# Performance work log

Hardware: AMD Instinct MI355X
Metric: run time of the kernel (lower is better)

## Reference

```python
import jax, jax.numpy as jnp
import numpy as np

N_AGT, N_CTX, E, D, NC = 100000, 10000, 1000000, 128, 2


def _gn(x, w, b, eps=1e-5):
    # GroupNorm(num_groups=1) on (N, C): normalize over channels, affine.
    m = jnp.mean(x, axis=-1, keepdims=True)
    v = jnp.mean((x - m) ** 2, axis=-1, keepdims=True)
    return (x - m) * jax.lax.rsqrt(v + eps) * w + b


def setup_inputs() -> dict:
    key = jax.random.key(0)
    ks = jax.random.split(key, 16)
    s = 0.05  # weight scale
    return {
        "agts": jax.random.normal(ks[0], (N_AGT, D), jnp.float32),
        "ctx": jax.random.normal(ks[1], (N_CTX, D), jnp.float32),
        "agt_ctrs": jax.random.normal(ks[2], (N_AGT, NC), jnp.float32),
        "ctx_ctrs": jax.random.normal(ks[3], (N_CTX, NC), jnp.float32),
        "hi": jax.random.randint(ks[4], (E,), 0, N_AGT, jnp.int32),
        "wi": jax.random.randint(ks[5], (E,), 0, N_CTX, jnp.int32),
        "dist_w1": jax.random.normal(ks[6], (D, NC), jnp.float32) * s,
        "dist_b1": jnp.zeros((D,), jnp.float32),
        "dist_w2": jax.random.normal(ks[7], (D, D), jnp.float32) * s,
        "dist_gw": jnp.ones((D,), jnp.float32),
        "dist_gb": jnp.zeros((D,), jnp.float32),
        "q_w": jax.random.normal(ks[8], (D, D), jnp.float32) * s,
        "q_gw": jnp.ones((D,), jnp.float32),
        "q_gb": jnp.zeros((D,), jnp.float32),
        "ctx_w1": jax.random.normal(ks[9], (D, 3 * D), jnp.float32) * s,
        "ctx_gw": jnp.ones((D,), jnp.float32),
        "ctx_gb": jnp.zeros((D,), jnp.float32),
        "ctx_w2": jax.random.normal(ks[10], (D, D), jnp.float32) * s,
        "agt_w": jax.random.normal(ks[11], (D, D), jnp.float32) * s,
        "norm_gw": jnp.ones((D,), jnp.float32),
        "norm_gb": jnp.zeros((D,), jnp.float32),
        "lin_w": jax.random.normal(ks[12], (D, D), jnp.float32) * s,
        "lin_gw": jnp.ones((D,), jnp.float32),
        "lin_gb": jnp.zeros((D,), jnp.float32),
    }


def reference(agts, ctx, agt_ctrs, ctx_ctrs, hi, wi,
              dist_w1, dist_b1, dist_w2, dist_gw, dist_gb,
              q_w, q_gw, q_gb,
              ctx_w1, ctx_gw, ctx_gb, ctx_w2,
              agt_w, norm_gw, norm_gb,
              lin_w, lin_gw, lin_gb):
    res = agts
    # per-edge relative displacement: [E, 2]
    d = agt_ctrs[hi] - ctx_ctrs[wi]
    # dist MLP: Linear(2,128)+ReLU, Linear(128,128,nobias)+GN+ReLU
    d = jax.nn.relu(d @ dist_w1.T + dist_b1)
    d = jax.nn.relu(_gn(d @ dist_w2.T, dist_gw, dist_gb))
    # query: Linear(128,128,nobias)+GN+ReLU on gathered agents
    q = jax.nn.relu(_gn(agts[hi] @ q_w.T, q_gw, q_gb))
    # concat-MLP over edges: [E, 384] -> [E, 128]
    c = jnp.concatenate([d, q, ctx[wi]], axis=1)
    c = jax.nn.relu(_gn(c @ ctx_w1.T, ctx_gw, ctx_gb))
    c = c @ ctx_w2.T
    # agent transform + index_add scatter of edge messages
    a = agts @ agt_w.T
    a = a.at[hi].add(c)
    a = jax.nn.relu(_gn(a, norm_gw, norm_gb))
    a = _gn(a @ lin_w.T, lin_gw, lin_gb)  # Linear block with act=False
    a = jax.nn.relu(a + res)
    return a
```

## Files before the change

kernel.cpp:

```cpp
#include <hip/hip_runtime.h>
#include <stdint.h>


#define N_AGT 100000
#define N_CTX 10000
#define NE    1000000
#define D     128

typedef __attribute__((ext_vector_type(8))) __bf16 bf16x8;
typedef __attribute__((ext_vector_type(4))) float f32x4;
typedef __attribute__((ext_vector_type(4))) unsigned int uint32x4;
typedef __attribute__((ext_vector_type(8))) unsigned short ushort8;

__device__ __forceinline__ float bf_lo(uint32_t u){ return __uint_as_float(u << 16); }
__device__ __forceinline__ float bf_hi(uint32_t u){ return __uint_as_float(u & 0xFFFF0000u); }
__device__ __forceinline__ uint16_t f2bf(float f){
  uint32_t u = __float_as_uint(f);
  u += 0x7FFFu + ((u >> 16) & 1u);
  return (uint16_t)(u >> 16);
}
__device__ __forceinline__ float bf2f(uint16_t v){ return __uint_as_float(((uint32_t)v) << 16); }

__device__ __forceinline__ f32x4 mfma16(bf16x8 a, bf16x8 b, f32x4 c){
  return __builtin_amdgcn_mfma_f32_16x16x32_bf16(a, b, c, 0, 0, 0);
}

__device__ __forceinline__ void wave_lgkm0(){
  asm volatile("s_waitcnt lgkmcnt(0)" ::: "memory");
  __builtin_amdgcn_sched_barrier(0);
}


__device__ __forceinline__ void stage_wsz(char* dst, const float* __restrict__ W,
                                          int rs, int co, int tid, int nthr){
  for (int idx = tid; idx < 128*16; idx += nthr){
    const int row = idx >> 4, ch = idx & 15;
    const float4 f0 = *(const float4*)(W + (size_t)row*rs + co + ch*8);
    const float4 f1 = *(const float4*)(W + (size_t)row*rs + co + ch*8 + 4);
    ushort8 u;
    u[0]=f2bf(f0.x); u[1]=f2bf(f0.y); u[2]=f2bf(f0.z); u[3]=f2bf(f0.w);
    u[4]=f2bf(f1.x); u[5]=f2bf(f1.y); u[6]=f2bf(f1.z); u[7]=f2bf(f1.w);
    *(uint32x4*)(dst + row*256 + ((ch*16) ^ ((row&7)<<4))) = __builtin_bit_cast(uint32x4, u);
  }
}

__device__ __forceinline__ bf16x8 ldfrag(const char* base, int row, int cb){
  return __builtin_bit_cast(bf16x8,
      *(const uint32x4*)(base + row*256 + (cb ^ ((row&7)<<4))));
}

__global__ __launch_bounds__(256) void k_hist(const int* __restrict__ hi,
                                              int* __restrict__ cnt){
  for (int i = blockIdx.x*256 + threadIdx.x; i < NE; i += gridDim.x*256)
    atomicAdd(&cnt[hi[i]], 1);
}

__global__ __launch_bounds__(1024) void k_scan(int* __restrict__ cnt){
  __shared__ int part[1024];
  const int t = threadIdx.x;
  const int chunk = (N_AGT + 1023) / 1024;
  const int lo = t*chunk, hi2 = min(lo + chunk, N_AGT);
  int s = 0;
  for (int i = lo; i < hi2; i++) s += cnt[i];
  part[t] = s;
  __syncthreads();
  for (int ofs = 1; ofs < 1024; ofs <<= 1){
    int add = (t >= ofs) ? part[t - ofs] : 0;
    __syncthreads();
    part[t] += add;
    __syncthreads();
  }
  int run = part[t] - s;
  for (int i = lo; i < hi2; i++){
    const int c = cnt[i];
    cnt[i] = run;
    run += c;
  }
}

__global__ __launch_bounds__(256) void k_scatter(const int* __restrict__ hi,
                                                 const int* __restrict__ wi,
                                                 int* __restrict__ cur,
                                                 int* __restrict__ hs,
                                                 int* __restrict__ ws){
  for (int i = blockIdx.x*256 + threadIdx.x; i < NE; i += gridDim.x*256){
    const int h = hi[i];
    const int pos = atomicAdd(&cur[h], 1);
    hs[pos] = h;
    ws[pos] = wi[i];
  }
}

#define NWIT (NE/16)

__device__ __forceinline__ void mm16(const char* T, const char* W,
                                     int llo, int lhi, f32x4 acc[8]){
  bf16x8 a[4];
  #pragma unroll
  for (int kt = 0; kt < 4; kt++) a[kt] = ldfrag(T, llo, kt*64 + lhi*16);
  #pragma unroll
  for (int nt = 0; nt < 8; nt++){
    acc[nt] = (f32x4)0.f;
    #pragma unroll
    for (int kt = 0; kt < 4; kt++){
      const bf16x8 b = ldfrag(W, nt*16 + llo, kt*64 + lhi*16);
      acc[nt] = mfma16(a[kt], b, acc[nt]);
    }
  }
}

__device__ __forceinline__ void gn_reg(f32x4 acc[8], const float gw[8],
                                       const float gb[8]){
  float s[4] = {0,0,0,0}, ss[4] = {0,0,0,0};
  #pragma unroll
  for (int nt = 0; nt < 8; nt++)
    #pragma unroll
    for (int r = 0; r < 4; r++){
      const float v = acc[nt][r];
      s[r] += v; ss[r] += v*v;
    }
  #pragma unroll
  for (int m = 1; m < 16; m <<= 1)
    #pragma unroll
    for (int r = 0; r < 4; r++){
      s[r] += __shfl_xor(s[r], m);
      ss[r] += __shfl_xor(ss[r], m);
    }
  float mean[4], rstd[4];
  #pragma unroll
  for (int r = 0; r < 4; r++){
    mean[r] = s[r]*(1.f/128.f);
    const float var = ss[r]*(1.f/128.f) - mean[r]*mean[r];
    rstd[r] = rsqrtf(var + 1e-5f);
  }
  #pragma unroll
  for (int nt = 0; nt < 8; nt++)
    #pragma unroll
    for (int r = 0; r < 4; r++)
      acc[nt][r] = fmaxf((acc[nt][r]-mean[r])*rstd[r]*gw[nt] + gb[nt], 0.f);
}

__device__ __forceinline__ void scat16(char* T, const f32x4 acc[8],
                                       int llo, int lhi){
  #pragma unroll
  for (int nt = 0; nt < 8; nt++)
    #pragma unroll
    for (int r = 0; r < 4; r++){
      const int row = lhi*4 + r;
      *(uint16_t*)(T + row*256 + ((2*(nt*16 + llo)) ^ ((row&7)<<4))) =
          f2bf(acc[nt][r]);
    }
}

__global__ __launch_bounds__(512, 2) void k_edge_mfma(
    const float* __restrict__ agt_ctrs, const float* __restrict__ ctx_ctrs,
    const int* __restrict__ hs, const int* __restrict__ ws,
    const float* __restrict__ dist_w1, const float* __restrict__ dist_b1,
    const float* __restrict__ dist_gw, const float* __restrict__ dist_gb,
    const float* __restrict__ ctx_gw, const float* __restrict__ ctx_gb,
    const float* __restrict__ dist_w2, const float* __restrict__ ctx_w1,
    const float* __restrict__ ctx_w2,
    const uint16_t* __restrict__ QW, const uint16_t* __restrict__ CtxP,
    float* __restrict__ A0){
  extern __shared__ __align__(16) char smem[];
  const int tid  = threadIdx.x;
  const int wave = tid >> 6, lane = tid & 63;
  const int lhi  = lane >> 4, llo = lane & 15;

  stage_wsz(smem,         dist_w2, 128, 0, tid, 512);
  stage_wsz(smem + 32768, ctx_w1,  384, 0, tid, 512);
  stage_wsz(smem + 65536, ctx_w2,  128, 0, tid, 512);

  char* T = smem + 98304 + wave*4096;

  const int c0 = llo*8;
  float w1x[8], w1y[8], b1v[8];
  #pragma unroll
  for (int j = 0; j < 8; j++){
    w1x[j] = dist_w1[(c0+j)*2 + 0];
    w1y[j] = dist_w1[(c0+j)*2 + 1];
    b1v[j] = dist_b1[c0+j];
  }
  float dgwr[8], dgbr[8], cgwr[8], cgbr[8];
  #pragma unroll
  for (int nt = 0; nt < 8; nt++){
    dgwr[nt] = dist_gw[nt*16 + llo]; dgbr[nt] = dist_gb[nt*16 + llo];
    cgwr[nt] = ctx_gw[nt*16 + llo];  cgbr[nt] = ctx_gb[nt*16 + llo];
  }
  __syncthreads();

  const int wid = blockIdx.x*8 + wave;
  const int nw  = gridDim.x*8;

  for (int i = wid; i < NWIT; i += nw){
    const int base = i*16;
    const int4 h4 = *(const int4*)&hs[base + lhi*4];
    const int4 w4 = *(const int4*)&ws[base + lhi*4];
    const int hh[4] = {h4.x, h4.y, h4.z, h4.w};
    const int ww[4] = {w4.x, w4.y, w4.z, w4.w};
    const int h2 = hs[base + llo], w2 = ws[base + llo];
    uint32x4 qql[4], qcl[4];
    #pragma unroll
    for (int k = 0; k < 4; k++){
      qql[k] = *(const uint32x4*)&QW  [(size_t)h2*D + lhi*32 + k*8];
      qcl[k] = *(const uint32x4*)&CtxP[(size_t)w2*D + lhi*32 + k*8];
    }
    #pragma unroll
    for (int j = 0; j < 4; j++){
      const float2 ac = *(const float2*)&agt_ctrs[(size_t)hh[j]*2];
      const float2 cc = *(const float2*)&ctx_ctrs[(size_t)ww[j]*2];
      const float dx = ac.x - cc.x, dy = ac.y - cc.y;
      ushort8 u;
      #pragma unroll
      for (int c = 0; c < 8; c++)
        u[c] = f2bf(fmaxf(fmaf(dx, w1x[c], fmaf(dy, w1y[c], b1v[c])), 0.f));
      const int row = lhi*4 + j;
      *(uint32x4*)(T + row*256 + ((llo*16) ^ ((row&7)<<4))) =
          __builtin_bit_cast(uint32x4, u);
    }
    wave_lgkm0();
    f32x4 acc[8];
    mm16(T, smem, llo, lhi, acc);
    gn_reg(acc, dgwr, dgbr);
    wave_lgkm0();
    scat16(T, acc, llo, lhi);
    wave_lgkm0();
    mm16(T, smem + 32768, llo, lhi, acc);
    ushort8 qs[4];
    #pragma unroll
    for (int k = 0; k < 4; k++){
      const ushort8 a = __builtin_bit_cast(ushort8, qql[k]);
      const ushort8 b = __builtin_bit_cast(ushort8, qcl[k]);
      ushort8 v;
      #pragma unroll
      for (int j = 0; j < 8; j++) v[j] = f2bf(bf2f(a[j]) + bf2f(b[j]));
      qs[k] = v;
    }
    wave_lgkm0();
    #pragma unroll
    for (int k = 0; k < 4; k++)
      *(uint32x4*)(T + llo*256 + (((lhi*64) + k*16) ^ ((llo&7)<<4))) =
          __builtin_bit_cast(uint32x4, qs[k]);
    wave_lgkm0();
    #pragma unroll
    for (int nt = 0; nt < 8; nt++)
      #pragma unroll
      for (int r = 0; r < 4; r++){
        const int row = lhi*4 + r;
        const uint16_t q = *(const uint16_t*)(T + row*256 +
            ((2*(nt*16 + llo)) ^ ((row&7)<<4)));
        acc[nt][r] += bf2f(q);
      }
    gn_reg(acc, cgwr, cgbr);
    wave_lgkm0();
    scat16(T, acc, llo, lhi);
    wave_lgkm0();
    mm16(T, smem + 65536, llo, lhi, acc);
    wave_lgkm0();
    scat16(T, acc, llo, lhi);
    wave_lgkm0();
    {
      const int cA = lane, cB = lane + 64;
      float runA = 0.f, runB = 0.f;
      int hprev = __shfl(h2, 0);
      #pragma unroll
      for (int k = 0; k < 16; k++){
        const int hk = __shfl(h2, k);
        if (hk != hprev){
          atomicAdd(&A0[(size_t)hprev*D + cA], runA);
          atomicAdd(&A0[(size_t)hprev*D + cB], runB);
          runA = 0.f; runB = 0.f; hprev = hk;
        }
        runA += bf2f(*(const uint16_t*)(T + k*256 + ((2*cA) ^ ((k&7)<<4))));
        runB += bf2f(*(const uint16_t*)(T + k*256 + ((2*cB) ^ ((k&7)<<4))));
      }
      atomicAdd(&A0[(size_t)hprev*D + cA], runA);
      atomicAdd(&A0[(size_t)hprev*D + cB], runB);
    }
  }
}

__device__ __forceinline__ void mm_stage(const char* xb, const char* wm, int wv,
                                         int llo, int lhi, f32x4 acc[3][2]){
  #pragma unroll
  for (int kt = 0; kt < 4; kt++){
    const int cb = kt*64 + lhi*16;
    const bf16x8 b0 = ldfrag(wm, wv*32 + llo,      cb);
    const bf16x8 b1 = ldfrag(wm, wv*32 + 16 + llo, cb);
    #pragma unroll
    for (int mt = 0; mt < 3; mt++){
      const bf16x8 a = ldfrag(xb, mt*16 + llo, cb);
      acc[mt][0] = mfma16(a, b0, acc[mt][0]);
      acc[mt][1] = mfma16(a, b1, acc[mt][1]);
    }
  }
}

__device__ __forceinline__ void scat_acc(char* xb, const f32x4 acc[3][2],
                                         int wv, int llo, int lhi){
  #pragma unroll
  for (int mt = 0; mt < 3; mt++)
    #pragma unroll
    for (int ntl = 0; ntl < 2; ntl++)
      #pragma unroll
      for (int r = 0; r < 4; r++){
        const int m = mt*16 + lhi*4 + r;
        const int n = wv*32 + ntl*16 + llo;
        *(uint16_t*)(xb + m*256 + ((n*2) ^ ((m&7)<<4))) = f2bf(acc[mt][ntl][r]);
      }
}

__device__ __forceinline__ void gn_rowpass(char* xb, const int rr[3], int llo,
                                           const float gw[8], const float gb[8]){
  #pragma unroll
  for (int i = 0; i < 3; i++){
    const int row = rr[i];
    char* p = xb + row*256 + ((llo*16) ^ ((row&7)<<4));
    ushort8 u = __builtin_bit_cast(ushort8, *(const uint32x4*)p);
    float f[8]; float s = 0.f, ss = 0.f;
    #pragma unroll
    for (int j = 0; j < 8; j++){ f[j] = bf2f(u[j]); s += f[j]; ss += f[j]*f[j]; }
    #pragma unroll
    for (int m = 1; m < 16; m <<= 1){ s += __shfl_xor(s, m); ss += __shfl_xor(ss, m); }
    const float mean = s*(1.f/128.f);
    const float var  = ss*(1.f/128.f) - mean*mean;
    const float rstd = rsqrtf(var + 1e-5f);
    #pragma unroll
    for (int j = 0; j < 8; j++){
      const float g = fmaxf((f[j]-mean)*rstd*gw[j] + gb[j], 0.f);
      u[j] = f2bf(g);
    }
    *(uint32x4*)p = __builtin_bit_cast(uint32x4, u);
  }
}

#define NITER_A ((N_AGT + 95) / 96)

__global__ __launch_bounds__(512, 2) void k_agent_pre_mfma(
    const float* __restrict__ agts, const float* __restrict__ q_w,
    const float* __restrict__ ctx_w1, const float* __restrict__ agt_w,
    const float* __restrict__ q_gw, const float* __restrict__ q_gb,
    uint16_t* __restrict__ QW, float* __restrict__ A0){
  extern __shared__ __align__(16) char smem[];
  const int tid  = threadIdx.x;
  const int wave = tid >> 6, lane = tid & 63;
  const int grp  = wave >> 2, wv = wave & 3;
  const int lhi  = lane >> 4, llo = lane & 15;

  stage_wsz(smem,         q_w,    128, 0,   tid, 512);
  stage_wsz(smem + 32768, agt_w,  128, 0,   tid, 512);
  stage_wsz(smem + 65536, ctx_w1, 384, 128, tid, 512);

  char* xb = smem + 98304 + grp*12288;
  const int c0 = llo*8;
  float qgw[8], qgb[8];
  #pragma unroll
  for (int j = 0; j < 8; j++){ qgw[j] = q_gw[c0+j]; qgb[j] = q_gb[c0+j]; }
  __syncthreads();

  const int tg = tid & 255;
  int rr[3];
  #pragma unroll
  for (int i = 0; i < 3; i++) rr[i] = wv*12 + i*4 + lhi;

  for (int it = blockIdx.x; it < NITER_A; it += gridDim.x){
    const int rbase = it*96 + grp*48;
    for (int idx = tg; idx < 48*32; idx += 256){
      const int row = idx >> 5, c4 = idx & 31;
      int gr = rbase + row; if (gr >= N_AGT) gr = N_AGT - 1;
      const float4 f = *(const float4*)(agts + (size_t)gr*D + c4*4);
      const uint32_t lo = ((uint32_t)f2bf(f.y) << 16) | (uint32_t)f2bf(f.x);
      const uint32_t hi2 = ((uint32_t)f2bf(f.w) << 16) | (uint32_t)f2bf(f.z);
      *(uint2*)(xb + row*256 + ((c4*8) ^ ((row&7)<<4))) = make_uint2(lo, hi2);
    }
    __syncthreads();
    f32x4 acc[3][2];
    #pragma unroll
    for (int mt = 0; mt < 3; mt++){ acc[mt][0] = (f32x4)0.f; acc[mt][1] = (f32x4)0.f; }
    mm_stage(xb, smem + 32768, wv, llo, lhi, acc);
    #pragma unroll
    for (int mt = 0; mt < 3; mt++)
      #pragma unroll
      for (int ntl = 0; ntl < 2; ntl++)
        #pragma unroll
        for (int r = 0; r < 4; r++){
          const int m = mt*16 + lhi*4 + r;
          if (rbase + m < N_AGT){
            const int n = wv*32 + ntl*16 + llo;
            A0[(size_t)(rbase + m)*D + n] = acc[mt][ntl][r];
          }
        }
    #pragma unroll
    for (int mt = 0; mt < 3; mt++){ acc[mt][0] = (f32x4)0.f; acc[mt][1] = (f32x4)0.f; }
    mm_stage(xb, smem, wv, llo, lhi, acc);
    __syncthreads();
    scat_acc(xb, acc, wv, llo, lhi);
    __syncthreads();
    gn_rowpass(xb, rr, llo, qgw, qgb);
    __syncthreads();
    #pragma unroll
    for (int mt = 0; mt < 3; mt++){ acc[mt][0] = (f32x4)0.f; acc[mt][1] = (f32x4)0.f; }
    mm_stage(xb, smem + 65536, wv, llo, lhi, acc);
    __syncthreads();
    scat_acc(xb, acc, wv, llo, lhi);
    __syncthreads();
    #pragma unroll
    for (int i = 0; i < 3; i++){
      const int row = rr[i], gr = rbase + row;
      if (gr < N_AGT){
        const uint32x4 u = *(const uint32x4*)(xb + row*256 + ((llo*16) ^ ((row&7)<<4)));
        *(uint32x4*)(QW + (size_t)gr*D + c0) = u;
      }
    }
    __syncthreads();
  }
}

__global__ __launch_bounds__(512, 4) void k_post_mfma(
    float* __restrict__ A0, const float* __restrict__ agts,
    const float* __restrict__ lin_w,
    const float* __restrict__ norm_gw, const float* __restrict__ norm_gb,
    const float* __restrict__ lin_gw, const float* __restrict__ lin_gb){
  extern __shared__ __align__(16) char smem[];
  const int tid  = threadIdx.x;
  const int wave = tid >> 6, lane = tid & 63;
  const int grp  = wave >> 2, wv = wave & 3;
  const int lhi  = lane >> 4, llo = lane & 15;

  stage_wsz(smem, lin_w, 128, 0, tid, 512);
  char* xb = smem + 32768 + grp*12288;
  const int c0 = llo*8;
  float ngw[8], ngb[8], lgw[8], lgb[8];
  #pragma unroll
  for (int j = 0; j < 8; j++){
    ngw[j] = norm_gw[c0+j]; ngb[j] = norm_gb[c0+j];
    lgw[j] = lin_gw[c0+j];  lgb[j] = lin_gb[c0+j];
  }
  __syncthreads();

  int rr[3];
  #pragma unroll
  for (int i = 0; i < 3; i++) rr[i] = wv*12 + i*4 + lhi;

  for (int it = blockIdx.x; it < NITER_A; it += gridDim.x){
    const int rbase = it*96 + grp*48;
    #pragma unroll
    for (int i = 0; i < 3; i++){
      const int row = rr[i];
      int gr = rbase + row; if (gr >= N_AGT) gr = N_AGT - 1;
      const float4 a0 = *(const float4*)(A0 + (size_t)gr*D + c0);
      const float4 a1 = *(const float4*)(A0 + (size_t)gr*D + c0 + 4);
      float f[8] = {a0.x,a0.y,a0.z,a0.w,a1.x,a1.y,a1.z,a1.w};
      float s = 0.f, ss = 0.f;
      #pragma unroll
      for (int j = 0; j < 8; j++){ s += f[j]; ss += f[j]*f[j]; }
      #pragma unroll
      for (int m = 1; m < 16; m <<= 1){ s += __shfl_xor(s, m); ss += __shfl_xor(ss, m); }
      const float mean = s*(1.f/128.f);
      const float var  = ss*(1.f/128.f) - mean*mean;
      const float rstd = rsqrtf(var + 1e-5f);
      ushort8 u;
      #pragma unroll
      for (int j = 0; j < 8; j++)
        u[j] = f2bf(fmaxf((f[j]-mean)*rstd*ngw[j] + ngb[j], 0.f));
      *(uint32x4*)(xb + row*256 + ((llo*16) ^ ((row&7)<<4))) =
          __builtin_bit_cast(uint32x4, u);
    }
    __syncthreads();
    f32x4 acc[3][2];
    #pragma unroll
    for (int mt = 0; mt < 3; mt++){ acc[mt][0] = (f32x4)0.f; acc[mt][1] = (f32x4)0.f; }
    mm_stage(xb, smem, wv, llo, lhi, acc);
    __syncthreads();
    scat_acc(xb, acc, wv, llo, lhi);
    __syncthreads();
    #pragma unroll
    for (int i = 0; i < 3; i++){
      const int row = rr[i];
      const char* p = xb + row*256 + ((llo*16) ^ ((row&7)<<4));
      const ushort8 u = __builtin_bit_cast(ushort8, *(const uint32x4*)p);
      float f[8]; float s = 0.f, ss = 0.f;
      #pragma unroll
      for (int j = 0; j < 8; j++){ f[j] = bf2f(u[j]); s += f[j]; ss += f[j]*f[j]; }
      #pragma unroll
      for (int m = 1; m < 16; m <<= 1){ s += __shfl_xor(s, m); ss += __shfl_xor(ss, m); }
      const float mean = s*(1.f/128.f);
      const float var  = ss*(1.f/128.f) - mean*mean;
      const float rstd = rsqrtf(var + 1e-5f);
      const int gr = rbase + row;
      if (gr < N_AGT){
        const float4 r0 = *(const float4*)(agts + (size_t)gr*D + c0);
        const float4 r1 = *(const float4*)(agts + (size_t)gr*D + c0 + 4);
        const float res[8] = {r0.x,r0.y,r0.z,r0.w,r1.x,r1.y,r1.z,r1.w};
        float o[8];
        float4 o0, o1;
        #pragma unroll
        for (int j = 0; j < 8; j++)
          o[j] = fmaxf((f[j]-mean)*rstd*lgw[j] + lgb[j] + res[j], 0.f);
        o0.x=o[0]; o0.y=o[1]; o0.z=o[2]; o0.w=o[3];
        o1.x=o[4]; o1.y=o[5]; o1.z=o[6]; o1.w=o[7];
        *(float4*)(A0 + (size_t)gr*D + c0)     = o0;
        *(float4*)(A0 + (size_t)gr*D + c0 + 4) = o1;
      }
    }
    __syncthreads();
  }
}

__device__ __forceinline__ void stage_w4(uint32_t* wp, const float* __restrict__ W,
                                         int rs, int co, int tid, int nthr){
  for (int idx = tid; idx < 32*128; idx += nthr){
    int p2 = idx & 31, o = idx >> 5;
    const float4 f = *(const float4*)(W + (size_t)o*rs + co + p2*4);
    uint32_t lo = ((uint32_t)f2bf(f.y) << 16) | (uint32_t)f2bf(f.x);
    uint32_t hi = ((uint32_t)f2bf(f.w) << 16) | (uint32_t)f2bf(f.z);
    *(uint2*)&wp[(p2*128 + o)*2] = make_uint2(lo, hi);
  }
}

__device__ __forceinline__ float dot128(const uint32_t* wp, const float* xb, int o){
  float acc = 0.f;
  #pragma unroll 8
  for (int p2 = 0; p2 < 32; p2++){
    const uint2 w = *(const uint2*)&wp[(p2*128 + o)*2];
    const float4 x = *(const float4*)&xb[p2*4];
    acc += x.x*bf_lo(w.x) + x.y*bf_hi(w.x) + x.z*bf_lo(w.y) + x.w*bf_hi(w.y);
  }
  return acc;
}

__global__ __launch_bounds__(128) void k_ctx(const float* __restrict__ ctx,
                                             const float* __restrict__ ctx_w1,
                                             uint16_t* __restrict__ CtxP){
  __shared__ __align__(16) uint32_t wc[32*128*2];
  __shared__ __align__(16) float xbuf[128];
  const int tid = threadIdx.x;
  stage_w4(wc, ctx_w1, 384, 256, tid, 128);
  __syncthreads();
  for (int row = blockIdx.x; row < N_CTX; row += gridDim.x){
    __syncthreads();
    xbuf[tid] = ctx[(size_t)row*D + tid];
    __syncthreads();
    const float acc = dot128(wc, xbuf, tid);
    CtxP[(size_t)row*D + tid] = f2bf(acc);
  }
}

extern "C" void kernel_launch(void* const* d_in, const int* in_sizes, int n_in,
                              void* d_out, int out_size, void* d_ws, size_t ws_size,
                              hipStream_t stream){
  const float* agts     = (const float*)d_in[0];
  const float* ctx      = (const float*)d_in[1];
  const float* agt_ctrs = (const float*)d_in[2];
  const float* ctx_ctrs = (const float*)d_in[3];
  const int*   hi       = (const int*)d_in[4];
  const int*   wi       = (const int*)d_in[5];
  const float* dist_w1  = (const float*)d_in[6];
  const float* dist_b1  = (const float*)d_in[7];
  const float* dist_w2  = (const float*)d_in[8];
  const float* dist_gw  = (const float*)d_in[9];
  const float* dist_gb  = (const float*)d_in[10];
  const float* q_w      = (const float*)d_in[11];
  const float* q_gw     = (const float*)d_in[12];
  const float* q_gb     = (const float*)d_in[13];
  const float* ctx_w1   = (const float*)d_in[14];
  const float* ctx_gw   = (const float*)d_in[15];
  const float* ctx_gb   = (const float*)d_in[16];
  const float* ctx_w2   = (const float*)d_in[17];
  const float* agt_w    = (const float*)d_in[18];
  const float* norm_gw  = (const float*)d_in[19];
  const float* norm_gb  = (const float*)d_in[20];
  const float* lin_w    = (const float*)d_in[21];
  const float* lin_gw   = (const float*)d_in[22];
  const float* lin_gb   = (const float*)d_in[23];

  uint16_t* QW   = (uint16_t*)d_ws;
  uint16_t* CtxP = QW + (size_t)N_AGT * D;
  int*      cnt  = (int*)((char*)d_ws + 28160000);
  int*      hs   = (int*)((char*)d_ws + 28560000);
  int*      wss  = (int*)((char*)d_ws + 32560000);
  float*    A0   = (float*)d_out;

  const int EDGE_LDS = 131072;
  const int APRE_LDS = 122880;
  const int POST_LDS = 57344;
  hipFuncSetAttribute((const void*)k_edge_mfma,
                      hipFuncAttributeMaxDynamicSharedMemorySize, EDGE_LDS);
  hipFuncSetAttribute((const void*)k_agent_pre_mfma,
                      hipFuncAttributeMaxDynamicSharedMemorySize, APRE_LDS);
  hipFuncSetAttribute((const void*)k_post_mfma,
                      hipFuncAttributeMaxDynamicSharedMemorySize, POST_LDS);

  hipMemsetAsync(cnt, 0, (size_t)N_AGT*4, stream);
  k_hist<<<2048, 256, 0, stream>>>(hi, cnt);
  k_scan<<<1, 1024, 0, stream>>>(cnt);
  k_scatter<<<2048, 256, 0, stream>>>(hi, wi, cnt, hs, wss);

  k_ctx<<<1024, 128, 0, stream>>>(ctx, ctx_w1, CtxP);
  k_agent_pre_mfma<<<256, 512, APRE_LDS, stream>>>(agts, q_w, ctx_w1, agt_w,
      q_gw, q_gb, QW, A0);
  k_edge_mfma<<<256, 512, EDGE_LDS, stream>>>(agt_ctrs, ctx_ctrs, hs, wss,
      dist_w1, dist_b1, dist_gw, dist_gb, ctx_gw, ctx_gb,
      dist_w2, ctx_w1, ctx_w2, QW, CtxP, A0);
  k_post_mfma<<<512, 512, POST_LDS, stream>>>(A0, agts, lin_w,
      norm_gw, norm_gb, lin_gw, lin_gb);
}
```

Before: 726.5 us.

## Parallelize CSR scan, pack edge index pairs, use hardware bf16 conversion

Replaces the single-block 100k-element prefix scan with a three-kernel multi-block scan (block sums, scan of sums, local scan). Packs the sorted (h,w) index pairs into one 64-bit array so the edge kernel fetches both with fewer loads. Swaps the manual round-to-nearest-even float-to-bf16 conversion for the compiler's native __bf16 cast in the hot edge loop. The scan change adds two extra kernel launches, and the native cast may round NaN and edge cases differently from the manual version.

```diff
diff --git a/kernel.cpp b/kernel.cpp
--- a/kernel.cpp
+++ b/kernel.cpp
@@ -18,6 +18,10 @@
   uint32_t u = __float_as_uint(f);
   u += 0x7FFFu + ((u >> 16) & 1u);
   return (uint16_t)(u >> 16);
+}
+__device__ __forceinline__ uint16_t f2bf_fast(float f){
+  const __bf16 b = (__bf16)f;
+  return __builtin_bit_cast(uint16_t, b);
 }
 __device__ __forceinline__ float bf2f(uint16_t v){ return __uint_as_float(((uint32_t)v) << 16); }
 
@@ -49,29 +53,63 @@
       *(const uint32x4*)(base + row*256 + (cb ^ ((row&7)<<4))));
 }
 
+#define SCAN_B  256
+#define SCAN_CH ((N_AGT + SCAN_B - 1) / SCAN_B)
+
 __global__ __launch_bounds__(256) void k_hist(const int* __restrict__ hi,
                                               int* __restrict__ cnt){
   for (int i = blockIdx.x*256 + threadIdx.x; i < NE; i += gridDim.x*256)
     atomicAdd(&cnt[hi[i]], 1);
 }
 
-__global__ __launch_bounds__(1024) void k_scan(int* __restrict__ cnt){
-  __shared__ int part[1024];
+__global__ __launch_bounds__(256) void k_scan1(const int* __restrict__ cnt,
+                                               int* __restrict__ bsum){
+  __shared__ int red[4];
+  const int b = blockIdx.x, t = threadIdx.x;
+  const int lo = b*SCAN_CH, hiX = min(lo + SCAN_CH, N_AGT);
+  int s = 0;
+  for (int i = lo + t; i < hiX; i += 256) s += cnt[i];
+  #pragma unroll
+  for (int m = 1; m < 64; m <<= 1) s += __shfl_xor(s, m);
+  if ((t & 63) == 0) red[t >> 6] = s;
+  __syncthreads();
+  if (t == 0) bsum[b] = red[0] + red[1] + red[2] + red[3];
+}
+
+__global__ __launch_bounds__(SCAN_B) void k_scan2(int* __restrict__ bsum){
+  __shared__ int part[SCAN_B];
   const int t = threadIdx.x;
-  const int chunk = (N_AGT + 1023) / 1024;
-  const int lo = t*chunk, hi2 = min(lo + chunk, N_AGT);
+  const int v = bsum[t];
+  part[t] = v;
+  __syncthreads();
+  for (int ofs = 1; ofs < SCAN_B; ofs <<= 1){
+    const int add = (t >= ofs) ? part[t - ofs] : 0;
+    __syncthreads();
+    part[t] += add;
+    __syncthreads();
+  }
+  bsum[t] = part[t] - v;
+}
+
+__global__ __launch_bounds__(256) void k_scan3(int* __restrict__ cnt,
+                                               const int* __restrict__ bsum){
+  __shared__ int tpart[256];
+  const int b = blockIdx.x, t = threadIdx.x;
+  const int lo = b*SCAN_CH, hiX = min(lo + SCAN_CH, N_AGT);
+  const int per = (SCAN_CH + 255) / 256;
+  const int s0 = lo + t*per, s1 = min(s0 + per, hiX);
   int s = 0;
-  for (int i = lo; i < hi2; i++) s += cnt[i];
-  part[t] = s;
+  for (int i = s0; i < s1; i++) s += cnt[i];
+  tpart[t] = s;
   __syncthreads();
-  for (int ofs = 1; ofs < 1024; ofs <<= 1){
-    int add = (t >= ofs) ? part[t - ofs] : 0;
-    __syncthreads();
-    part[t] += add;
-    __syncthreads();
-  }
-  int run = part[t] - s;
-  for (int i = lo; i < hi2; i++){
+  for (int ofs = 1; ofs < 256; ofs <<= 1){
+    const int add = (t >= ofs) ? tpart[t - ofs] : 0;
+    __syncthreads();
+    tpart[t] += add;
+    __syncthreads();
+  }
+  int run = bsum[b] + tpart[t] - s;
+  for (int i = s0; i < s1; i++){
     const int c = cnt[i];
     cnt[i] = run;
     run += c;
@@ -81,13 +119,11 @@
 __global__ __launch_bounds__(256) void k_scatter(const int* __restrict__ hi,
                                                  const int* __restrict__ wi,
                                                  int* __restrict__ cur,
-                                                 int* __restrict__ hs,
-                                                 int* __restrict__ ws){
+                                                 uint64_t* __restrict__ hw){
   for (int i = blockIdx.x*256 + threadIdx.x; i < NE; i += gridDim.x*256){
     const int h = hi[i];
     const int pos = atomicAdd(&cur[h], 1);
-    hs[pos] = h;
-    ws[pos] = wi[i];
+    hw[pos] = ((uint64_t)(uint32_t)wi[i] << 32) | (uint32_t)h;
   }
 }
 
@@ -148,13 +184,13 @@
     for (int r = 0; r < 4; r++){
       const int row = lhi*4 + r;
       *(uint16_t*)(T + row*256 + ((2*(nt*16 + llo)) ^ ((row&7)<<4))) =
-          f2bf(acc[nt][r]);
+          f2bf_fast(acc[nt][r]);
     }
 }
 
 __global__ __launch_bounds__(512, 2) void k_edge_mfma(
     const float* __restrict__ agt_ctrs, const float* __restrict__ ctx_ctrs,
-    const int* __restrict__ hs, const int* __restrict__ ws,
+    const uint32_t* __restrict__ hw32,
     const float* __restrict__ dist_w1, const float* __restrict__ dist_b1,
     const float* __restrict__ dist_gw, const float* __restrict__ dist_gb,
     const float* __restrict__ ctx_gw, const float* __restrict__ ctx_gb,
@@ -194,11 +230,12 @@
 
   for (int i = wid; i < NWIT; i += nw){
     const int base = i*16;
-    const int4 h4 = *(const int4*)&hs[base + lhi*4];
-    const int4 w4 = *(const int4*)&ws[base + lhi*4];
-    const int hh[4] = {h4.x, h4.y, h4.z, h4.w};
-    const int ww[4] = {w4.x, w4.y, w4.z, w4.w};
-    const int h2 = hs[base + llo], w2 = ws[base + llo];
+    const uint32x4 q0 = *(const uint32x4*)&hw32[2*(base + lhi*4)];
+    const uint32x4 q1 = *(const uint32x4*)&hw32[2*(base + lhi*4) + 4];
+    const int hh[4] = {(int)q0[0], (int)q0[2], (int)q1[0], (int)q1[2]};
+    const int ww[4] = {(int)q0[1], (int)q0[3], (int)q1[1], (int)q1[3]};
+    const uint2 p2 = *(const uint2*)&hw32[2*(base + llo)];
+    const int h2 = (int)p2.x, w2 = (int)p2.y;
     uint32x4 qql[4], qcl[4];
     #pragma unroll
     for (int k = 0; k < 4; k++){
@@ -213,7 +250,7 @@
       ushort8 u;
       #pragma unroll
       for (int c = 0; c < 8; c++)
-        u[c] = f2bf(fmaxf(fmaf(dx, w1x[c], fmaf(dy, w1y[c], b1v[c])), 0.f));
+        u[c] = f2bf_fast(fmaxf(fmaf(dx, w1x[c], fmaf(dy, w1y[c], b1v[c])), 0.f));
       const int row = lhi*4 + j;
       *(uint32x4*)(T + row*256 + ((llo*16) ^ ((row&7)<<4))) =
           __builtin_bit_cast(uint32x4, u);
@@ -233,7 +270,7 @@
       const ushort8 b = __builtin_bit_cast(ushort8, qcl[k]);
       ushort8 v;
       #pragma unroll
-      for (int j = 0; j < 8; j++) v[j] = f2bf(bf2f(a[j]) + bf2f(b[j]));
+      for (int j = 0; j < 8; j++) v[j] = f2bf_fast(bf2f(a[j]) + bf2f(b[j]));
       qs[k] = v;
     }
     wave_lgkm0();
@@ -577,8 +614,8 @@
   uint16_t* QW   = (uint16_t*)d_ws;
   uint16_t* CtxP = QW + (size_t)N_AGT * D;
   int*      cnt  = (int*)((char*)d_ws + 28160000);
-  int*      hs   = (int*)((char*)d_ws + 28560000);
-  int*      wss  = (int*)((char*)d_ws + 32560000);
+  int*      bsum = (int*)((char*)d_ws + 28560000);
+  uint64_t* hw   = (uint64_t*)((char*)d_ws + 28561024);
   float*    A0   = (float*)d_out;
 
   const int EDGE_LDS = 131072;
@@ -593,13 +630,16 @@
 
   hipMemsetAsync(cnt, 0, (size_t)N_AGT*4, stream);
   k_hist<<<2048, 256, 0, stream>>>(hi, cnt);
-  k_scan<<<1, 1024, 0, stream>>>(cnt);
-  k_scatter<<<2048, 256, 0, stream>>>(hi, wi, cnt, hs, wss);
+  k_scan1<<<SCAN_B, 256, 0, stream>>>(cnt, bsum);
+  k_scan2<<<1, SCAN_B, 0, stream>>>(bsum);
+  k_scan3<<<SCAN_B, 256, 0, stream>>>(cnt, bsum);
+  k_scatter<<<2048, 256, 0, stream>>>(hi, wi, cnt, hw);
 
   k_ctx<<<1024, 128, 0, stream>>>(ctx, ctx_w1, CtxP);
   k_agent_pre_mfma<<<256, 512, APRE_LDS, stream>>>(agts, q_w, ctx_w1, agt_w,
       q_gw, q_gb, QW, A0);
-  k_edge_mfma<<<256, 512, EDGE_LDS, stream>>>(agt_ctrs, ctx_ctrs, hs, wss,
+  k_edge_mfma<<<256, 512, EDGE_LDS, stream>>>(agt_ctrs, ctx_ctrs,
+      (const uint32_t*)hw,
       dist_w1, dist_b1, dist_gw, dist_gb, ctx_gw, ctx_gb,
       dist_w2, ctx_w1, ctx_w2, QW, CtxP, A0);
   k_post_mfma<<<512, 512, POST_LDS, stream>>>(A0, agts, lin_w,
```

Result: faster. 581.4 us, median of 3 (-20.0%).
